# Performance work log

Hardware: AMD Instinct MI355X
Metric: run time of the kernel (lower is better)

Reference implementation:

```python
import jax, jax.numpy as jnp
import numpy as np

N_NODES = 100000
N_EDGES = 1600000


def sage_conv(x, src, dst, W_self, W_neigh, b):
    # mean aggregation over incoming neighbors (DGL SAGEConv 'mean')
    msg = x[src]  # [E, d] gather
    agg = jax.ops.segment_sum(msg, dst, num_segments=N_NODES)
    deg = jax.ops.segment_sum(jnp.ones((src.shape[0],), x.dtype), dst, num_segments=N_NODES)
    h_neigh = agg / jnp.maximum(deg, 1.0)[:, None]
    return x @ W_self + h_neigh @ W_neigh + b


def setup_inputs() -> dict:
    key = jax.random.key(0)
    ks = jax.random.split(key, 9)
    x = jax.random.normal(ks[0], (N_NODES, 64), dtype=jnp.float32)
    src = jax.random.randint(ks[1], (N_EDGES,), 0, N_NODES)
    dst = jax.random.randint(ks[2], (N_EDGES,), 0, N_NODES)
    W_self1 = jax.random.normal(ks[3], (64, 32), dtype=jnp.float32) * 0.125
    W_neigh1 = jax.random.normal(ks[4], (64, 32), dtype=jnp.float32) * 0.125
    b1 = jnp.zeros((32,), jnp.float32)
    W_self2 = jax.random.normal(ks[5], (32, 16), dtype=jnp.float32) * 0.18
    W_neigh2 = jax.random.normal(ks[6], (32, 16), dtype=jnp.float32) * 0.18
    b2 = jnp.zeros((16,), jnp.float32)
    return {"x": x, "src": src, "dst": dst,
            "W_self1": W_self1, "W_neigh1": W_neigh1, "b1": b1,
            "W_self2": W_self2, "W_neigh2": W_neigh2, "b2": b2}


def reference(x, src, dst, W_self1, W_neigh1, b1, W_self2, W_neigh2, b2):
    h = sage_conv(x, src, dst, W_self1, W_neigh1, b1)   # [N, 32]
    h = sage_conv(h, src, dst, W_self2, W_neigh2, b2)   # [N, 16]
    return h
```

## Files before the change

kernel.cpp:

```cpp
#include <hip/hip_runtime.h>

#define NN 100000
#define NE 1600000
#define NPART 391
#define NC 391
#define CHUNK 4096
#define CAPB 4608
#define PROJ_NPB 64
#define PROJ_BLKS ((NN + PROJ_NPB - 1) / PROJ_NPB)

typedef float floatx2 __attribute__((ext_vector_type(2)));

__device__ __forceinline__ unsigned short f2bf(float f) {
    unsigned u = __float_as_uint(f);
    u = (u + 0x7FFFu + ((u >> 16) & 1u)) >> 16;
    return (unsigned short)u;
}
__device__ __forceinline__ float bflo(unsigned u) { return __uint_as_float(u << 16); }
__device__ __forceinline__ float bfhi(unsigned u) { return __uint_as_float(u & 0xFFFF0000u); }

__device__ __forceinline__ unsigned fp8enc(float f) {
    unsigned u = __float_as_uint(f);
    unsigned s = u >> 31;
    unsigned t = (u & 0x7FFFFFFFu) + 0x7FFFFu + ((u >> 20) & 1u);
    int e8 = (int)((t >> 23) & 255u) - 120;
    unsigned m = (t >> 20) & 7u;
    if (e8 <= 0) return s << 7;
    if (e8 > 15) { e8 = 15; m = 6; }
    return (s << 7) | ((unsigned)e8 << 3) | m;
}
__device__ __forceinline__ void acc8(float* a, uint2 v) {
    floatx2 p0 = __builtin_amdgcn_cvt_pk_f32_fp8(v.x, false);
    floatx2 p1 = __builtin_amdgcn_cvt_pk_f32_fp8(v.x, true);
    floatx2 p2 = __builtin_amdgcn_cvt_pk_f32_fp8(v.y, false);
    floatx2 p3 = __builtin_amdgcn_cvt_pk_f32_fp8(v.y, true);
    a[0] += p0[0]; a[1] += p0[1]; a[2] += p1[0]; a[3] += p1[1];
    a[4] += p2[0]; a[5] += p2[1]; a[6] += p3[0]; a[7] += p3[1];
}

__global__ __launch_bounds__(512) void bin_kernel(
    const int* __restrict__ src, const int* __restrict__ dst,
    unsigned* __restrict__ slots, int* __restrict__ cntCB, int* __restrict__ ofsCB)
{
    __shared__ int hist[NPART];
    __shared__ int scn[512];
    __shared__ int cur[NPART];
    __shared__ unsigned buf[CHUNK];
    const int tid = threadIdx.x;
    const int c = blockIdx.x;
    for (int i = tid; i < NPART; i += 512) hist[i] = 0;
    __syncthreads();
    const int e0 = c * CHUNK;
    const int e1 = (e0 + CHUNK < NE) ? e0 + CHUNK : NE;
    int      eb[8];
    unsigned pk[8];
#pragma unroll
    for (int u = 0; u < 8; ++u) {
        int e = e0 + tid + u * 512;
        if (e < e1) {
            int d = dst[e], s = src[e];
            eb[u] = d >> 8;
            pk[u] = ((unsigned)(d & 255) << 17) | (unsigned)s;
            atomicAdd(&hist[eb[u]], 1);
        } else eb[u] = -1;
    }
    __syncthreads();
    int v = (tid < NPART) ? hist[tid] : 0;
    scn[tid] = v;
    __syncthreads();
    for (int d = 1; d < 512; d <<= 1) {
        int u = (tid >= d) ? scn[tid - d] : 0;
        __syncthreads();
        scn[tid] += u;
        __syncthreads();
    }
    const int excl = scn[tid] - v;
    if (tid < NPART) {
        cur[tid] = excl;
        cntCB[(size_t)c * NPART + tid] = v;
        ofsCB[(size_t)c * NPART + tid] = excl;
    }
    __syncthreads();
#pragma unroll
    for (int u = 0; u < 8; ++u) {
        if (eb[u] >= 0) {
            int pos = atomicAdd(&cur[eb[u]], 1);
            buf[pos] = pk[u];
        }
    }
    __syncthreads();
    const int m = e1 - e0;
    unsigned* op = slots + (size_t)c * CHUNK;
    for (int i = tid; i < m; i += 512) op[i] = buf[i];
}

struct CsrSh {
    unsigned ech[CAPB];
    int s[512];
    int myofs[NC], ccnt[NC], gofs[NC];
    int cntl[256], scn[256], curl[256];
};
struct ProjSh {
    float Wcat[64 * 64];
    float bl[32];
    float4 Xl4[PROJ_NPB][17];
};

__global__ __launch_bounds__(512) void csrproj_kernel(
    const unsigned* __restrict__ slots, const int* __restrict__ cntCB,
    const int* __restrict__ ofsCB, int* __restrict__ off, int* __restrict__ esrc,
    const float* __restrict__ X, const float* __restrict__ Wn1,
    const float* __restrict__ Ws1, const float* __restrict__ b1,
    unsigned char* __restrict__ P1, unsigned short* __restrict__ P1s)
{
    __shared__ union { CsrSh c; ProjSh p; } sh;
    const int tid = threadIdx.x;
    if (blockIdx.x < NPART) {
        const int b = blockIdx.x;
        int v = (tid < NC) ? cntCB[(size_t)tid * NPART + b] : 0;
        sh.c.s[tid] = v;
        if (tid < NC) {
            sh.c.ccnt[tid] = v;
            sh.c.gofs[tid] = ofsCB[(size_t)tid * NPART + b];
        }
        __syncthreads();
        for (int d = 1; d < 512; d <<= 1) {
            int u = (tid >= d) ? sh.c.s[tid - d] : 0;
            __syncthreads();
            sh.c.s[tid] += u;
            __syncthreads();
        }
        if (tid < NC) sh.c.myofs[tid] = sh.c.s[tid] - v;
        __syncthreads();
        int total = sh.c.s[NC - 1];
        if (total > CAPB) total = CAPB;

        for (int idx = tid; idx < NC * 16; idx += 512) {
            int c = idx >> 4, k = idx & 15;
            if (k < sh.c.ccnt[c]) {
                int p = sh.c.myofs[c] + k;
                if (p < CAPB)
                    sh.c.ech[p] = slots[(size_t)c * CHUNK + sh.c.gofs[c] + k];
            }
        }
        if (tid < NC) {
            const int cnt = sh.c.ccnt[tid];
            const int d0  = sh.c.myofs[tid];
            const unsigned* sp = slots + (size_t)tid * CHUNK + sh.c.gofs[tid];
            for (int k = 16; k < cnt; ++k) {
                int p = d0 + k;
                if (p < CAPB) sh.c.ech[p] = sp[k];
            }
        }
        if (tid < 256) sh.c.cntl[tid] = 0;
        __syncthreads();

        for (int i = tid; i < total; i += 512) atomicAdd(&sh.c.cntl[sh.c.ech[i] >> 17], 1);
        __syncthreads();
        int nv = (tid < 256) ? sh.c.cntl[tid] : 0;
        if (tid < 256) sh.c.scn[tid] = nv;
        __syncthreads();
        for (int d = 1; d < 256; d <<= 1) {
            int u = (tid >= d && tid < 256) ? sh.c.scn[tid - d] : 0;
            __syncthreads();
            if (tid < 256) sh.c.scn[tid] += u;
            __syncthreads();
        }
        const int base  = b * CAPB;
        const int nbase = b << 8;
        const int nmax  = (NN - nbase < 256) ? (NN - nbase) : 256;
        if (tid < nmax) off[nbase + tid] = base + sh.c.scn[tid];
        if (tid < 256)  sh.c.curl[tid] = base + sh.c.scn[tid] - nv;
        __syncthreads();
        for (int i = tid; i < total; i += 512) {
            unsigned ev = sh.c.ech[i];
            int pos = atomicAdd(&sh.c.curl[ev >> 17], 1);
            esrc[pos] = (int)(ev & 0x1FFFFu);
        }
    } else {
        const int pb = blockIdx.x - NPART;
        const int nbase = pb * PROJ_NPB;
        for (int i = tid; i < 64 * 64; i += 512) {
            int k = i >> 6, j = i & 63;
            sh.p.Wcat[i] = (j < 32) ? Wn1[k * 32 + j] : Ws1[k * 32 + (j - 32)];
        }
        if (tid < 32) sh.p.bl[tid] = b1[tid];
        for (int i = tid; i < PROJ_NPB * 16; i += 512) {
            int ln = i >> 4, k4 = i & 15;
            int n = nbase + ln;
            float4 xv = {0.f, 0.f, 0.f, 0.f};
            if (n < NN) xv = *reinterpret_cast<const float4*>(X + (size_t)n * 64 + k4 * 4);
            sh.p.Xl4[ln][k4] = xv;
        }
        __syncthreads();
        const int j4 = tid & 15;
        const int nl = tid >> 4;
        const int n0 = nbase + nl * 2;
        const int n1 = n0 + 1;
        const float4* W4 = reinterpret_cast<const float4*>(sh.p.Wcat);
        float4 a0 = {0.f,0.f,0.f,0.f}, a1 = {0.f,0.f,0.f,0.f};
        for (int k4 = 0; k4 < 16; ++k4) {
            const float4 x0 = sh.p.Xl4[nl * 2][k4];
            const float4 x1 = sh.p.Xl4[nl * 2 + 1][k4];
            const float* x0p = (const float*)&x0;
            const float* x1p = (const float*)&x1;
#pragma unroll
            for (int kk = 0; kk < 4; ++kk) {
                const float4 w = W4[(k4 * 4 + kk) * 16 + j4];
                const float v0 = x0p[kk], v1 = x1p[kk];
                a0.x += v0 * w.x; a0.y += v0 * w.y; a0.z += v0 * w.z; a0.w += v0 * w.w;
                a1.x += v1 * w.x; a1.y += v1 * w.y; a1.z += v1 * w.z; a1.w += v1 * w.w;
            }
        }
        if (j4 < 8) {
            unsigned pk0 = fp8enc(a0.x) | (fp8enc(a0.y) << 8) |
                           (fp8enc(a0.z) << 16) | (fp8enc(a0.w) << 24);
            unsigned pk1 = fp8enc(a1.x) | (fp8enc(a1.y) << 8) |
                           (fp8enc(a1.z) << 16) | (fp8enc(a1.w) << 24);
            if (n0 < NN) *reinterpret_cast<unsigned*>(P1 + (size_t)n0 * 32 + j4 * 4) = pk0;
            if (n1 < NN) *reinterpret_cast<unsigned*>(P1 + (size_t)n1 * 32 + j4 * 4) = pk1;
        } else {
            const int jb = (j4 - 8) * 4;
            const float4 bb = {sh.p.bl[jb], sh.p.bl[jb+1], sh.p.bl[jb+2], sh.p.bl[jb+3]};
            uint2 o0, o1;
            o0.x = (unsigned)f2bf(a0.x + bb.x) | ((unsigned)f2bf(a0.y + bb.y) << 16);
            o0.y = (unsigned)f2bf(a0.z + bb.z) | ((unsigned)f2bf(a0.w + bb.w) << 16);
            o1.x = (unsigned)f2bf(a1.x + bb.x) | ((unsigned)f2bf(a1.y + bb.y) << 16);
            o1.y = (unsigned)f2bf(a1.z + bb.z) | ((unsigned)f2bf(a1.w + bb.w) << 16);
            unsigned* P1su = (unsigned*)P1s;
            if (n0 < NN) *reinterpret_cast<uint2*>(P1su + (size_t)n0 * 16 + (j4 - 8) * 2) = o0;
            if (n1 < NN) *reinterpret_cast<uint2*>(P1su + (size_t)n1 * 16 + (j4 - 8) * 2) = o1;
        }
    }
}

__global__ __launch_bounds__(256) void aggproj1_kernel(
    const unsigned* __restrict__ P1, const int* __restrict__ esrc,
    const int* __restrict__ off, const unsigned* __restrict__ P1s,
    const float* __restrict__ Wn2, const float* __restrict__ Ws2,
    const float* __restrict__ b2,
    unsigned* __restrict__ P2, unsigned* __restrict__ S2)
{
    __shared__ float W2l[32 * 16];
    __shared__ float W3l[32 * 16];
    __shared__ float b2l[16];
    __shared__ float accL[32][33];
    __shared__ float Hl[32][33];
    const int tid = threadIdx.x;
    const int nbase = blockIdx.x * 32;
    for (int i = tid; i < 32 * 16; i += 256) W2l[i] = Wn2[i];
    for (int i = tid; i < 32 * 16; i += 256) W3l[i] = Ws2[i];
    if (tid < 16) b2l[tid] = b2[tid];
    const int ln  = tid >> 3;
    const int q   = tid & 7;
    const int sub = q >> 2;
    const int f4  = q & 3;
    const int n   = nbase + ln;
    float a[8] = {0,0,0,0,0,0,0,0};
    int e0 = 0, e1 = 0;
    if (n < NN) {
        e0 = (n & 255) ? off[n - 1] : (n >> 8) * CAPB;
        e1 = off[n];
        int e = e0 + sub;
        for (; e + 14 < e1; e += 16) {
            int sA[8];
#pragma unroll
            for (int u = 0; u < 8; ++u) sA[u] = esrc[e + 2 * u];
            uint2 vA[8];
#pragma unroll
            for (int u = 0; u < 8; ++u)
                vA[u] = *reinterpret_cast<const uint2*>(P1 + (size_t)sA[u] * 8 + f4 * 2);
#pragma unroll
            for (int u = 0; u < 8; ++u) acc8(a, vA[u]);
        }
        for (; e + 6 < e1; e += 8) {
            int s0 = esrc[e], s1 = esrc[e+2], s2 = esrc[e+4], s3 = esrc[e+6];
            const uint2 v0 = *reinterpret_cast<const uint2*>(P1 + (size_t)s0 * 8 + f4 * 2);
            const uint2 v1 = *reinterpret_cast<const uint2*>(P1 + (size_t)s1 * 8 + f4 * 2);
            const uint2 v2 = *reinterpret_cast<const uint2*>(P1 + (size_t)s2 * 8 + f4 * 2);
            const uint2 v3 = *reinterpret_cast<const uint2*>(P1 + (size_t)s3 * 8 + f4 * 2);
            acc8(a, v0); acc8(a, v1); acc8(a, v2); acc8(a, v3);
        }
        for (; e < e1; e += 2) {
            int s0 = esrc[e];
            const uint2 v0 = *reinterpret_cast<const uint2*>(P1 + (size_t)s0 * 8 + f4 * 2);
            acc8(a, v0);
        }
    }
#pragma unroll
    for (int i = 0; i < 8; ++i) a[i] += __shfl_xor(a[i], 4);
    if (sub == 0) {
#pragma unroll
        for (int i = 0; i < 8; ++i) accL[ln][f4 * 8 + i] = a[i];
    }
    __syncthreads();
    float d = (float)(e1 - e0);
    if (d < 1.f) d = 1.f;
    const float inv = 1.f / d;
    float r[4] = {0.f, 0.f, 0.f, 0.f};
    if (n < NN) {
        const uint2 sp = *reinterpret_cast<const uint2*>(P1s + (size_t)n * 16 + q * 2);
        r[0] = accL[ln][q * 4 + 0] * inv + bflo(sp.x);
        r[1] = accL[ln][q * 4 + 1] * inv + bfhi(sp.x);
        r[2] = accL[ln][q * 4 + 2] * inv + bflo(sp.y);
        r[3] = accL[ln][q * 4 + 3] * inv + bfhi(sp.y);
    }
#pragma unroll
    for (int i = 0; i < 4; ++i) Hl[ln][q * 4 + i] = r[i];
    __syncthreads();
    const int j2 = q * 2;
    float p2[2] = {0.f, 0.f}, s2[2] = {b2l[j2], b2l[j2 + 1]};
#pragma unroll
    for (int k = 0; k < 32; ++k) {
        float hv = Hl[ln][k];
        p2[0] += hv * W2l[k * 16 + j2];
        p2[1] += hv * W2l[k * 16 + j2 + 1];
        s2[0] += hv * W3l[k * 16 + j2];
        s2[1] += hv * W3l[k * 16 + j2 + 1];
    }
    if (n < NN) {
        P2[(size_t)n * 8 + q] = (unsigned)f2bf(p2[0]) | ((unsigned)f2bf(p2[1]) << 16);
        S2[(size_t)n * 8 + q] = (unsigned)f2bf(s2[0]) | ((unsigned)f2bf(s2[1]) << 16);
    }
}

__global__ __launch_bounds__(256) void aggproj2_kernel(
    const unsigned* __restrict__ P2, const int* __restrict__ esrc,
    const int* __restrict__ off, const unsigned* __restrict__ S2,
    float* __restrict__ out)
{
    __shared__ float accL[32][17];
    const int tid = threadIdx.x;
    const int nbase = blockIdx.x * 32;
    const int ln  = tid >> 3;
    const int q   = tid & 7;
    const int sub = q >> 2;
    const int f4  = q & 3;
    const int n   = nbase + ln;
    float a[4] = {0.f, 0.f, 0.f, 0.f};
    int e0 = 0, e1 = 0;
    if (n < NN) {
        e0 = (n & 255) ? off[n - 1] : (n >> 8) * CAPB;
        e1 = off[n];
        int e = e0 + sub;
        for (; e + 14 < e1; e += 16) {
            int sA[8];
#pragma unroll
            for (int u = 0; u < 8; ++u) sA[u] = esrc[e + 2 * u];
            uint2 vA[8];
#pragma unroll
            for (int u = 0; u < 8; ++u)
                vA[u] = *reinterpret_cast<const uint2*>(P2 + (size_t)sA[u] * 8 + f4 * 2);
#pragma unroll
            for (int u = 0; u < 8; ++u) {
                a[0] += bflo(vA[u].x); a[1] += bfhi(vA[u].x);
                a[2] += bflo(vA[u].y); a[3] += bfhi(vA[u].y);
            }
        }
        for (; e + 6 < e1; e += 8) {
            int s0 = esrc[e], s1 = esrc[e+2], s2 = esrc[e+4], s3 = esrc[e+6];
            const uint2 v0 = *reinterpret_cast<const uint2*>(P2 + (size_t)s0 * 8 + f4 * 2);
            const uint2 v1 = *reinterpret_cast<const uint2*>(P2 + (size_t)s1 * 8 + f4 * 2);
            const uint2 v2 = *reinterpret_cast<const uint2*>(P2 + (size_t)s2 * 8 + f4 * 2);
            const uint2 v3 = *reinterpret_cast<const uint2*>(P2 + (size_t)s3 * 8 + f4 * 2);
            a[0] += bflo(v0.x) + bflo(v1.x) + bflo(v2.x) + bflo(v3.x);
            a[1] += bfhi(v0.x) + bfhi(v1.x) + bfhi(v2.x) + bfhi(v3.x);
            a[2] += bflo(v0.y) + bflo(v1.y) + bflo(v2.y) + bflo(v3.y);
            a[3] += bfhi(v0.y) + bfhi(v1.y) + bfhi(v2.y) + bfhi(v3.y);
        }
        for (; e < e1; e += 2) {
            int s0 = esrc[e];
            const uint2 v0 = *reinterpret_cast<const uint2*>(P2 + (size_t)s0 * 8 + f4 * 2);
            a[0] += bflo(v0.x); a[1] += bfhi(v0.x);
            a[2] += bflo(v0.y); a[3] += bfhi(v0.y);
        }
    }
#pragma unroll
    for (int i = 0; i < 4; ++i) a[i] += __shfl_xor(a[i], 4);
    if (sub == 0) {
#pragma unroll
        for (int i = 0; i < 4; ++i) accL[ln][f4 * 4 + i] = a[i];
    }
    __syncthreads();
    if (n >= NN) return;
    float d = (float)(e1 - e0);
    if (d < 1.f) d = 1.f;
    const float inv = 1.f / d;
    const int j2 = q * 2;
    const unsigned sv = S2[(size_t)n * 8 + q];
    float2 o;
    o.x = accL[ln][j2]     * inv + bflo(sv);
    o.y = accL[ln][j2 + 1] * inv + bfhi(sv);
    *reinterpret_cast<float2*>(out + (size_t)n * 16 + j2) = o;
}

extern "C" void kernel_launch(void* const* d_in, const int* in_sizes, int n_in,
                              void* d_out, int out_size, void* d_ws, size_t ws_size,
                              hipStream_t stream)
{
    const float* x   = (const float*)d_in[0];
    const int*   src = (const int*)d_in[1];
    const int*   dst = (const int*)d_in[2];
    const float* Ws1 = (const float*)d_in[3];
    const float* Wn1 = (const float*)d_in[4];
    const float* b1  = (const float*)d_in[5];
    const float* Ws2 = (const float*)d_in[6];
    const float* Wn2 = (const float*)d_in[7];
    const float* b2  = (const float*)d_in[8];
    float* out = (float*)d_out;

    char* ws = (char*)d_ws;
    int*            off   = (int*)(ws);
    int*            cntCB = (int*)(ws + (512u << 10));
    int*            ofsCB = (int*)(ws + (1152u << 10));
    int*            esrc  = (int*)(ws + (2u << 20));
    unsigned char*  P1    = (unsigned char*)(ws + (10u << 20));
    unsigned short* P1s   = (unsigned short*)(ws + (14u << 20));
    unsigned*       P2    = (unsigned*)(ws + (24u << 20));
    unsigned*       S2    = (unsigned*)(ws + (28u << 20));
    unsigned*       slots = (unsigned*)(ws + (40u << 20));

    bin_kernel<<<NC, 512, 0, stream>>>(src, dst, slots, cntCB, ofsCB);
    csrproj_kernel<<<NPART + PROJ_BLKS, 512, 0, stream>>>(
        slots, cntCB, ofsCB, off, esrc, x, Wn1, Ws1, b1, P1, P1s);
    aggproj1_kernel<<<(NN + 31) / 32, 256, 0, stream>>>(
        (const unsigned*)P1, esrc, off, (const unsigned*)P1s, Wn2, Ws2, b2, P2, S2);
    aggproj2_kernel<<<(NN + 31) / 32, 256, 0, stream>>>(
        P2, esrc, off, S2, out);
}
```

Measured before the change: 84.06 us.

## Split layer-1 projection blocks between the binning and CSR-build kernels

Merges the edge-binning kernel with part of the layer-1 dense projection, so bin blocks and projection blocks share one launch. The remaining projection blocks stay in the CSR-build kernel. The intent is to balance work across the two launches and fill idle CUs during the small 391-block binning pass. The shared-memory union now includes the projection tile, which may lower the occupancy of the bin blocks.

```diff
diff --git a/kernel.cpp b/kernel.cpp
--- a/kernel.cpp
+++ b/kernel.cpp
@@ -8,6 +8,8 @@
 #define CAPB 4608
 #define PROJ_NPB 64
 #define PROJ_BLKS ((NN + PROJ_NPB - 1) / PROJ_NPB)
+#define PH1 782
+#define PH2 (PROJ_BLKS - PH1)
 
 typedef float floatx2 __attribute__((ext_vector_type(2)));
 
@@ -38,62 +40,12 @@
     a[4] += p2[0]; a[5] += p2[1]; a[6] += p3[0]; a[7] += p3[1];
 }
 
-__global__ __launch_bounds__(512) void bin_kernel(
-    const int* __restrict__ src, const int* __restrict__ dst,
-    unsigned* __restrict__ slots, int* __restrict__ cntCB, int* __restrict__ ofsCB)
-{
-    __shared__ int hist[NPART];
-    __shared__ int scn[512];
-    __shared__ int cur[NPART];
-    __shared__ unsigned buf[CHUNK];
-    const int tid = threadIdx.x;
-    const int c = blockIdx.x;
-    for (int i = tid; i < NPART; i += 512) hist[i] = 0;
-    __syncthreads();
-    const int e0 = c * CHUNK;
-    const int e1 = (e0 + CHUNK < NE) ? e0 + CHUNK : NE;
-    int      eb[8];
-    unsigned pk[8];
-#pragma unroll
-    for (int u = 0; u < 8; ++u) {
-        int e = e0 + tid + u * 512;
-        if (e < e1) {
-            int d = dst[e], s = src[e];
-            eb[u] = d >> 8;
-            pk[u] = ((unsigned)(d & 255) << 17) | (unsigned)s;
-            atomicAdd(&hist[eb[u]], 1);
-        } else eb[u] = -1;
-    }
-    __syncthreads();
-    int v = (tid < NPART) ? hist[tid] : 0;
-    scn[tid] = v;
-    __syncthreads();
-    for (int d = 1; d < 512; d <<= 1) {
-        int u = (tid >= d) ? scn[tid - d] : 0;
-        __syncthreads();
-        scn[tid] += u;
-        __syncthreads();
-    }
-    const int excl = scn[tid] - v;
-    if (tid < NPART) {
-        cur[tid] = excl;
-        cntCB[(size_t)c * NPART + tid] = v;
-        ofsCB[(size_t)c * NPART + tid] = excl;
-    }
-    __syncthreads();
-#pragma unroll
-    for (int u = 0; u < 8; ++u) {
-        if (eb[u] >= 0) {
-            int pos = atomicAdd(&cur[eb[u]], 1);
-            buf[pos] = pk[u];
-        }
-    }
-    __syncthreads();
-    const int m = e1 - e0;
-    unsigned* op = slots + (size_t)c * CHUNK;
-    for (int i = tid; i < m; i += 512) op[i] = buf[i];
-}
-
+struct BinSh {
+    int hist[NPART];
+    int scn[512];
+    int cur[NPART];
+    unsigned buf[CHUNK];
+};
 struct CsrSh {
     unsigned ech[CAPB];
     int s[512];
@@ -106,6 +58,126 @@
     float4 Xl4[PROJ_NPB][17];
 };
 
+__device__ __forceinline__ void proj_body(
+    int pb, int tid, ProjSh& p,
+    const float* __restrict__ X, const float* __restrict__ Wn1,
+    const float* __restrict__ Ws1, const float* __restrict__ b1,
+    unsigned char* __restrict__ P1, unsigned short* __restrict__ P1s)
+{
+    const int nbase = pb * PROJ_NPB;
+    for (int i = tid; i < 64 * 64; i += 512) {
+        int k = i >> 6, j = i & 63;
+        p.Wcat[i] = (j < 32) ? Wn1[k * 32 + j] : Ws1[k * 32 + (j - 32)];
+    }
+    if (tid < 32) p.bl[tid] = b1[tid];
+    for (int i = tid; i < PROJ_NPB * 16; i += 512) {
+        int ln = i >> 4, k4 = i & 15;
+        int n = nbase + ln;
+        float4 xv = {0.f, 0.f, 0.f, 0.f};
+        if (n < NN) xv = *reinterpret_cast<const float4*>(X + (size_t)n * 64 + k4 * 4);
+        p.Xl4[ln][k4] = xv;
+    }
+    __syncthreads();
+    const int j4 = tid & 15;
+    const int nl = tid >> 4;
+    const int n0 = nbase + nl * 2;
+    const int n1 = n0 + 1;
+    const float4* W4 = reinterpret_cast<const float4*>(p.Wcat);
+    float4 a0 = {0.f,0.f,0.f,0.f}, a1 = {0.f,0.f,0.f,0.f};
+    for (int k4 = 0; k4 < 16; ++k4) {
+        const float4 x0 = p.Xl4[nl * 2][k4];
+        const float4 x1 = p.Xl4[nl * 2 + 1][k4];
+        const float* x0p = (const float*)&x0;
+        const float* x1p = (const float*)&x1;
+#pragma unroll
+        for (int kk = 0; kk < 4; ++kk) {
+            const float4 w = W4[(k4 * 4 + kk) * 16 + j4];
+            const float v0 = x0p[kk], v1 = x1p[kk];
+            a0.x += v0 * w.x; a0.y += v0 * w.y; a0.z += v0 * w.z; a0.w += v0 * w.w;
+            a1.x += v1 * w.x; a1.y += v1 * w.y; a1.z += v1 * w.z; a1.w += v1 * w.w;
+        }
+    }
+    if (j4 < 8) {
+        unsigned pk0 = fp8enc(a0.x) | (fp8enc(a0.y) << 8) |
+                       (fp8enc(a0.z) << 16) | (fp8enc(a0.w) << 24);
+        unsigned pk1 = fp8enc(a1.x) | (fp8enc(a1.y) << 8) |
+                       (fp8enc(a1.z) << 16) | (fp8enc(a1.w) << 24);
+        if (n0 < NN) *reinterpret_cast<unsigned*>(P1 + (size_t)n0 * 32 + j4 * 4) = pk0;
+        if (n1 < NN) *reinterpret_cast<unsigned*>(P1 + (size_t)n1 * 32 + j4 * 4) = pk1;
+    } else {
+        const int jb = (j4 - 8) * 4;
+        const float4 bb = {p.bl[jb], p.bl[jb+1], p.bl[jb+2], p.bl[jb+3]};
+        uint2 o0, o1;
+        o0.x = (unsigned)f2bf(a0.x + bb.x) | ((unsigned)f2bf(a0.y + bb.y) << 16);
+        o0.y = (unsigned)f2bf(a0.z + bb.z) | ((unsigned)f2bf(a0.w + bb.w) << 16);
+        o1.x = (unsigned)f2bf(a1.x + bb.x) | ((unsigned)f2bf(a1.y + bb.y) << 16);
+        o1.y = (unsigned)f2bf(a1.z + bb.z) | ((unsigned)f2bf(a1.w + bb.w) << 16);
+        unsigned* P1su = (unsigned*)P1s;
+        if (n0 < NN) *reinterpret_cast<uint2*>(P1su + (size_t)n0 * 16 + (j4 - 8) * 2) = o0;
+        if (n1 < NN) *reinterpret_cast<uint2*>(P1su + (size_t)n1 * 16 + (j4 - 8) * 2) = o1;
+    }
+}
+
+__global__ __launch_bounds__(512) void binproj_kernel(
+    const int* __restrict__ src, const int* __restrict__ dst,
+    unsigned* __restrict__ slots, int* __restrict__ cntCB, int* __restrict__ ofsCB,
+    const float* __restrict__ X, const float* __restrict__ Wn1,
+    const float* __restrict__ Ws1, const float* __restrict__ b1,
+    unsigned char* __restrict__ P1, unsigned short* __restrict__ P1s)
+{
+    __shared__ union { BinSh b; ProjSh p; } sh;
+    const int tid = threadIdx.x;
+    if (blockIdx.x < NC) {
+        const int c = blockIdx.x;
+        for (int i = tid; i < NPART; i += 512) sh.b.hist[i] = 0;
+        __syncthreads();
+        const int e0 = c * CHUNK;
+        const int e1 = (e0 + CHUNK < NE) ? e0 + CHUNK : NE;
+        int      eb[8];
+        unsigned pk[8];
+#pragma unroll
+        for (int u = 0; u < 8; ++u) {
+            int e = e0 + tid + u * 512;
+            if (e < e1) {
+                int d = dst[e], s = src[e];
+                eb[u] = d >> 8;
+                pk[u] = ((unsigned)(d & 255) << 17) | (unsigned)s;
+                atomicAdd(&sh.b.hist[eb[u]], 1);
+            } else eb[u] = -1;
+        }
+        __syncthreads();
+        int v = (tid < NPART) ? sh.b.hist[tid] : 0;
+        sh.b.scn[tid] = v;
+        __syncthreads();
+        for (int d = 1; d < 512; d <<= 1) {
+            int u = (tid >= d) ? sh.b.scn[tid - d] : 0;
+            __syncthreads();
+            sh.b.scn[tid] += u;
+            __syncthreads();
+        }
+        const int excl = sh.b.scn[tid] - v;
+        if (tid < NPART) {
+            sh.b.cur[tid] = excl;
+            cntCB[(size_t)c * NPART + tid] = v;
+            ofsCB[(size_t)c * NPART + tid] = excl;
+        }
+        __syncthreads();
+#pragma unroll
+        for (int u = 0; u < 8; ++u) {
+            if (eb[u] >= 0) {
+                int pos = atomicAdd(&sh.b.cur[eb[u]], 1);
+                sh.b.buf[pos] = pk[u];
+            }
+        }
+        __syncthreads();
+        const int m = e1 - e0;
+        unsigned* op = slots + (size_t)c * CHUNK;
+        for (int i = tid; i < m; i += 512) op[i] = sh.b.buf[i];
+    } else {
+        proj_body(blockIdx.x - NC, tid, sh.p, X, Wn1, Ws1, b1, P1, P1s);
+    }
+}
+
 __global__ __launch_bounds__(512) void csrproj_kernel(
     const unsigned* __restrict__ slots, const int* __restrict__ cntCB,
     const int* __restrict__ ofsCB, int* __restrict__ off, int* __restrict__ esrc,
@@ -178,59 +250,7 @@
             esrc[pos] = (int)(ev & 0x1FFFFu);
         }
     } else {
-        const int pb = blockIdx.x - NPART;
-        const int nbase = pb * PROJ_NPB;
-        for (int i = tid; i < 64 * 64; i += 512) {
-            int k = i >> 6, j = i & 63;
-            sh.p.Wcat[i] = (j < 32) ? Wn1[k * 32 + j] : Ws1[k * 32 + (j - 32)];
-        }
-        if (tid < 32) sh.p.bl[tid] = b1[tid];
-        for (int i = tid; i < PROJ_NPB * 16; i += 512) {
-            int ln = i >> 4, k4 = i & 15;
-            int n = nbase + ln;
-            float4 xv = {0.f, 0.f, 0.f, 0.f};
-            if (n < NN) xv = *reinterpret_cast<const float4*>(X + (size_t)n * 64 + k4 * 4);
-            sh.p.Xl4[ln][k4] = xv;
-        }
-        __syncthreads();
-        const int j4 = tid & 15;
-        const int nl = tid >> 4;
-        const int n0 = nbase + nl * 2;
-        const int n1 = n0 + 1;
-        const float4* W4 = reinterpret_cast<const float4*>(sh.p.Wcat);
-        float4 a0 = {0.f,0.f,0.f,0.f}, a1 = {0.f,0.f,0.f,0.f};
-        for (int k4 = 0; k4 < 16; ++k4) {
-            const float4 x0 = sh.p.Xl4[nl * 2][k4];
-            const float4 x1 = sh.p.Xl4[nl * 2 + 1][k4];
-            const float* x0p = (const float*)&x0;
-            const float* x1p = (const float*)&x1;
-#pragma unroll
-            for (int kk = 0; kk < 4; ++kk) {
-                const float4 w = W4[(k4 * 4 + kk) * 16 + j4];
-                const float v0 = x0p[kk], v1 = x1p[kk];
-                a0.x += v0 * w.x; a0.y += v0 * w.y; a0.z += v0 * w.z; a0.w += v0 * w.w;
-                a1.x += v1 * w.x; a1.y += v1 * w.y; a1.z += v1 * w.z; a1.w += v1 * w.w;
-            }
-        }
-        if (j4 < 8) {
-            unsigned pk0 = fp8enc(a0.x) | (fp8enc(a0.y) << 8) |
-                           (fp8enc(a0.z) << 16) | (fp8enc(a0.w) << 24);
-            unsigned pk1 = fp8enc(a1.x) | (fp8enc(a1.y) << 8) |
-                           (fp8enc(a1.z) << 16) | (fp8enc(a1.w) << 24);
-            if (n0 < NN) *reinterpret_cast<unsigned*>(P1 + (size_t)n0 * 32 + j4 * 4) = pk0;
-            if (n1 < NN) *reinterpret_cast<unsigned*>(P1 + (size_t)n1 * 32 + j4 * 4) = pk1;
-        } else {
-            const int jb = (j4 - 8) * 4;
-            const float4 bb = {sh.p.bl[jb], sh.p.bl[jb+1], sh.p.bl[jb+2], sh.p.bl[jb+3]};
-            uint2 o0, o1;
-            o0.x = (unsigned)f2bf(a0.x + bb.x) | ((unsigned)f2bf(a0.y + bb.y) << 16);
-            o0.y = (unsigned)f2bf(a0.z + bb.z) | ((unsigned)f2bf(a0.w + bb.w) << 16);
-            o1.x = (unsigned)f2bf(a1.x + bb.x) | ((unsigned)f2bf(a1.y + bb.y) << 16);
-            o1.y = (unsigned)f2bf(a1.z + bb.z) | ((unsigned)f2bf(a1.w + bb.w) << 16);
-            unsigned* P1su = (unsigned*)P1s;
-            if (n0 < NN) *reinterpret_cast<uint2*>(P1su + (size_t)n0 * 16 + (j4 - 8) * 2) = o0;
-            if (n1 < NN) *reinterpret_cast<uint2*>(P1su + (size_t)n1 * 16 + (j4 - 8) * 2) = o1;
-        }
+        proj_body(PH1 + (int)blockIdx.x - NPART, tid, sh.p, X, Wn1, Ws1, b1, P1, P1s);
     }
 }
 
@@ -420,8 +440,9 @@
     unsigned*       S2    = (unsigned*)(ws + (28u << 20));
     unsigned*       slots = (unsigned*)(ws + (40u << 20));
 
-    bin_kernel<<<NC, 512, 0, stream>>>(src, dst, slots, cntCB, ofsCB);
-    csrproj_kernel<<<NPART + PROJ_BLKS, 512, 0, stream>>>(
+    binproj_kernel<<<NC + PH1, 512, 0, stream>>>(
+        src, dst, slots, cntCB, ofsCB, x, Wn1, Ws1, b1, P1, P1s);
+    csrproj_kernel<<<NPART + PH2, 512, 0, stream>>>(
         slots, cntCB, ofsCB, off, esrc, x, Wn1, Ws1, b1, P1, P1s);
     aggproj1_kernel<<<(NN + 31) / 32, 256, 0, stream>>>(
         (const unsigned*)P1, esrc, off, (const unsigned*)P1s, Wn2, Ws2, b2, P2, S2);
```

New measurement: 86.76 us. 1.03x slower.
